# Performance work log

Hardware: AMD Instinct MI355X
Metric: run time of the kernel (lower is better)

Reference implementation:

```python
import jax, jax.numpy as jnp
import numpy as np
import math

N_LABELS = 63          # hard-coded in the original module (view(-1,63), range(63))
IN_DIMS = 8192
OUT_DIMS = 8192


def setup_inputs() -> dict:
    key = jax.random.key(0)
    k1, k2, k3 = jax.random.split(key, 3)
    Label = jax.random.normal(k1, (N_LABELS, IN_DIMS), dtype=jnp.float32)
    S = jax.random.uniform(k2, (N_LABELS, N_LABELS), dtype=jnp.float32)
    stdv = 1.0 / math.sqrt(IN_DIMS)
    # matches torch init: weight ~ U(-stdv, stdv), bias = 0
    W = jax.random.uniform(k3, (OUT_DIMS, IN_DIMS), dtype=jnp.float32,
                           minval=-stdv, maxval=stdv)
    b = jnp.zeros((OUT_DIMS,), dtype=jnp.float32)
    return {"Label": Label, "S": S, "W": W, "b": b}


def reference(Label, S, W, b):
    # MLP: Linear + ReLU -> (63, out_dims)
    X = jax.nn.relu(Label @ W.T + b)
    # torch .view(-1, 63): row-major reshape to (out_dims, 63) (NOT a transpose)
    ML = X.reshape(OUT_DIMS, N_LABELS)
    # loop i: new_Label[i, k] = sum_j S[i, j] * ML[k, j]  ==  S @ ML.T
    return jnp.einsum('ij,kj->ik', S, ML)  # (63, out_dims)
```

## Files before the change

kernel.cpp:

```cpp
#include <hip/hip_runtime.h>
#include <hip/hip_bf16.h>

#define IN_DIMS  8192
#define OUT_DIMS 8192
#define NLAB     63
#define KS       8
#define KCH      (IN_DIMS / KS)
#define BK       64
#define NT       (KCH / BK)
#define BN       64

#define BUFB     24576
#define AOFF     16384

typedef short  s16x8 __attribute__((ext_vector_type(8)));
typedef float  f32x4 __attribute__((ext_vector_type(4)));
typedef unsigned int u32;

__device__ __forceinline__ void gload16(const void* g, void* l) {
    __builtin_amdgcn_global_load_lds(
        (const __attribute__((address_space(1))) u32*)g,
        (__attribute__((address_space(3))) u32*)l, 16, 0, 0);
}

__device__ __forceinline__ unsigned int rne2(float a, float b) {
    unsigned int ua = __float_as_uint(a), ub = __float_as_uint(b);
    ua += 0x7FFFu + ((ua >> 16) & 1u);
    ub += 0x7FFFu + ((ub >> 16) & 1u);
    return (ua >> 16) | (ub & 0xFFFF0000u);
}

__device__ __forceinline__ s16x8 cvt8(float4 a, float4 b) {
    union { __hip_bfloat162 h[4]; s16x8 v; } u;
    u.h[0] = __float22bfloat162_rn(make_float2(a.x, a.y));
    u.h[1] = __float22bfloat162_rn(make_float2(a.z, a.w));
    u.h[2] = __float22bfloat162_rn(make_float2(b.x, b.y));
    u.h[3] = __float22bfloat162_rn(make_float2(b.z, b.w));
    return u.v;
}

__global__ __launch_bounds__(256) void k_prep(const float* __restrict__ L,
                                              unsigned short* __restrict__ A) {
    int e0 = (blockIdx.x * 256 + threadIdx.x) * 4;
    if (e0 >= 64 * IN_DIMS) return;
    float4 v = make_float4(0.f, 0.f, 0.f, 0.f);
    if (e0 < NLAB * IN_DIMS) v = *(const float4*)(L + e0);
    uint2 o;
    o.x = rne2(v.x, v.y);
    o.y = rne2(v.z, v.w);
    *(uint2*)(A + e0) = o;
}

__global__ __launch_bounds__(256, 3) void k_gemm(const float* __restrict__ W,
                                                 const unsigned short* __restrict__ A,
                                                 float* __restrict__ Xp) {
    extern __shared__ char lds[];
    const int nblk = blockIdx.x & 127;
    const int kspl = blockIdx.x >> 7;
    const int w    = threadIdx.x >> 6;
    const int l    = threadIdx.x & 63;
    const int r    = l & 15;
    const int g    = l >> 4;

    const int n0 = nblk * BN;

    f32x4 acc0 = {0,0,0,0}, acc1 = {0,0,0,0}, acc2 = {0,0,0,0}, acc3 = {0,0,0,0};

    auto stage = [&](int tt, int b) {
        const int k0 = kspl * KCH + tt * BK;
        char* base = lds + b * BUFB;
        #pragma unroll
        for (int i = 0; i < 4; ++i) {
            int j    = w * 4 + i;
            int row  = j * 4 + (l >> 4);
            int slot = (l & 15) ^ (row & 7);
            gload16(W + (long)(n0 + row) * IN_DIMS + k0 + slot * 4,
                    base + j * 1024 + l * 16);
        }
        #pragma unroll
        for (int i = 0; i < 2; ++i) {
            int j2   = w * 2 + i;
            int row  = j2 * 8 + (l >> 3);
            int slot = (l & 7) ^ (l >> 3);
            gload16(A + (long)row * IN_DIMS + k0 + slot * 8,
                    base + AOFF + j2 * 1024 + l * 16);
        }
    };

    stage(0, 0);

    for (int t = 0; t < NT; ++t) {
        if (t + 1 < NT) {
            stage(t + 1, (t + 1) & 1);
            asm volatile("s_waitcnt vmcnt(6)" ::: "memory");
        } else {
            asm volatile("s_waitcnt vmcnt(0)" ::: "memory");
        }
        __builtin_amdgcn_s_barrier();
        asm volatile("" ::: "memory");

        const char* base = lds + (t & 1) * BUFB;
        const float* ldsW = (const float*)base;
        const unsigned short* ldsA = (const unsigned short*)(base + AOFF);
        #pragma unroll
        for (int kk = 0; kk < 2; ++kk) {
            int rowb = w * 16 + r;
            int s0 = (kk * 8 + g * 2    ) ^ (r & 7);
            int s1 = (kk * 8 + g * 2 + 1) ^ (r & 7);
            float4 w0 = *(const float4*)(ldsW + rowb * 64 + s0 * 4);
            float4 w1 = *(const float4*)(ldsW + rowb * 64 + s1 * 4);
            s16x8 bw = cvt8(w0, w1);
            int sa = (kk * 4 + g) ^ (r & 7);
            s16x8 a0 = *(const s16x8*)(ldsA + ( 0 + r) * 64 + sa * 8);
            s16x8 a1 = *(const s16x8*)(ldsA + (16 + r) * 64 + sa * 8);
            s16x8 a2 = *(const s16x8*)(ldsA + (32 + r) * 64 + sa * 8);
            s16x8 a3 = *(const s16x8*)(ldsA + (48 + r) * 64 + sa * 8);
            acc0 = __builtin_amdgcn_mfma_f32_16x16x32_bf16(a0, bw, acc0, 0, 0, 0);
            acc1 = __builtin_amdgcn_mfma_f32_16x16x32_bf16(a1, bw, acc1, 0, 0, 0);
            acc2 = __builtin_amdgcn_mfma_f32_16x16x32_bf16(a2, bw, acc2, 0, 0, 0);
            acc3 = __builtin_amdgcn_mfma_f32_16x16x32_bf16(a3, bw, acc3, 0, 0, 0);
        }
        asm volatile("" ::: "memory");
        __builtin_amdgcn_s_barrier();
    }

    float* xo = Xp + (long)kspl * BN * OUT_DIMS + n0 + w * 16 + r;
    #pragma unroll
    for (int q = 0; q < 4; ++q) {
        int m = g * 4 + q;
        xo[(long)(m     ) * OUT_DIMS] = acc0[q];
        xo[(long)(m + 16) * OUT_DIMS] = acc1[q];
        xo[(long)(m + 32) * OUT_DIMS] = acc2[q];
        xo[(long)(m + 48) * OUT_DIMS] = acc3[q];
    }
}

__global__ __launch_bounds__(256) void k_out(const float* __restrict__ Xp,
                                             const float* __restrict__ S,
                                             const float* __restrict__ b,
                                             float* __restrict__ out) {
    __shared__ float sS[NLAB * NLAB];
    __shared__ float sml[64 * NLAB];
    const int k0 = blockIdx.x * 64;

    for (int p = threadIdx.x; p < NLAB * NLAB; p += 256) sS[p] = S[p];
    for (int p = threadIdx.x; p < 64 * NLAB; p += 256) {
        int gi = k0 * NLAB + p;
        float v = 0.f;
        #pragma unroll
        for (int s = 0; s < KS; ++s)
            v += Xp[(long)s * 64 * OUT_DIMS + gi];
        v += b[gi & (OUT_DIMS - 1)];
        sml[p] = v > 0.f ? v : 0.f;
    }
    __syncthreads();

    for (int p = threadIdx.x; p < NLAB * 64; p += 256) {
        int i  = p >> 6;
        int kk = p & 63;
        const float* srow = &sS[i * NLAB];
        const float* mrow = &sml[kk * NLAB];
        float sum = 0.f;
        #pragma unroll
        for (int j = 0; j < NLAB; ++j) sum += srow[j] * mrow[j];
        out[(long)i * OUT_DIMS + k0 + kk] = sum;
    }
}

extern "C" void kernel_launch(void* const* d_in, const int* in_sizes, int n_in,
                              void* d_out, int out_size, void* d_ws, size_t ws_size,
                              hipStream_t stream) {
    const float* Label = (const float*)d_in[0];
    const float* S     = (const float*)d_in[1];
    const float* W     = (const float*)d_in[2];
    const float* b     = (const float*)d_in[3];
    float* out = (float*)d_out;

    unsigned short* A  = (unsigned short*)d_ws;
    float*          Xp = (float*)((char*)d_ws + 64 * IN_DIMS * 2);

    k_prep<<<dim3((64 * IN_DIMS / 4 + 255) / 256), dim3(256), 0, stream>>>(Label, A);
    k_gemm<<<dim3(128 * KS), dim3(256), 2 * BUFB, stream>>>(W, A, Xp);
    k_out <<<dim3(OUT_DIMS / 64), dim3(256), 0, stream>>>(Xp, S, b, out);
}
```

Measured before the change: 92.00 us.

## Make GEMM waves independent: per-wave W staging, direct A loads, no barriers

Each wave now stages only its own 16 W rows into a private LDS region and reads the bf16 Label operand straight from global memory (L2-resident) instead of sharing it through LDS. This removes both block-wide barriers per k-step, shrinks LDS per block, and raises the occupancy hint to 4 blocks. The last iteration issues a dummy reload of tile 0 to keep a uniform vmcnt count. k_out now uses 32-column blocks for more parallelism. The risk is more global/L2 traffic for A, since every wave refetches it, and higher latency on those loads.

```diff
diff --git a/kernel.cpp b/kernel.cpp
--- a/kernel.cpp
+++ b/kernel.cpp
@@ -9,9 +9,8 @@
 #define BK       64
 #define NT       (KCH / BK)
 #define BN       64
-
-#define BUFB     24576
-#define AOFF     16384
+#define WAVETILE 4096
+#define BUFB     (4 * WAVETILE)
 
 typedef short  s16x8 __attribute__((ext_vector_type(8)));
 typedef float  f32x4 __attribute__((ext_vector_type(4)));
@@ -51,10 +50,10 @@
     *(uint2*)(A + e0) = o;
 }
 
-__global__ __launch_bounds__(256, 3) void k_gemm(const float* __restrict__ W,
+__global__ __launch_bounds__(256, 4) void k_gemm(const float* __restrict__ W,
                                                  const unsigned short* __restrict__ A,
                                                  float* __restrict__ Xp) {
-    extern __shared__ char lds[];
+    __shared__ char lds[2 * BUFB];
     const int nblk = blockIdx.x & 127;
     const int kspl = blockIdx.x >> 7;
     const int w    = threadIdx.x >> 6;
@@ -62,69 +61,59 @@
     const int r    = l & 15;
     const int g    = l >> 4;
 
-    const int n0 = nblk * BN;
+    const int  n0    = nblk * BN + w * 16;
+    const long kbase = (long)kspl * KCH;
+
+    char* wbuf0 = lds + w * WAVETILE;
+    char* wbuf1 = lds + BUFB + w * WAVETILE;
+
+    const int srow  = l >> 4;
+    const int sslot = l & 15;
+
+    auto stage = [&](int tt, char* buf) {
+        const long k0 = kbase + (long)tt * BK;
+        #pragma unroll
+        for (int i = 0; i < 4; ++i) {
+            int row  = i * 4 + srow;
+            int slot = sslot ^ (row & 7);
+            gload16(W + (long)(n0 + row) * IN_DIMS + k0 + slot * 4,
+                    buf + i * 1024 + l * 16);
+        }
+    };
+
+    stage(0, wbuf0);
+
+    const unsigned short* ap = A + (long)r * IN_DIMS + kbase + g * 8;
 
     f32x4 acc0 = {0,0,0,0}, acc1 = {0,0,0,0}, acc2 = {0,0,0,0}, acc3 = {0,0,0,0};
 
-    auto stage = [&](int tt, int b) {
-        const int k0 = kspl * KCH + tt * BK;
-        char* base = lds + b * BUFB;
-        #pragma unroll
-        for (int i = 0; i < 4; ++i) {
-            int j    = w * 4 + i;
-            int row  = j * 4 + (l >> 4);
-            int slot = (l & 15) ^ (row & 7);
-            gload16(W + (long)(n0 + row) * IN_DIMS + k0 + slot * 4,
-                    base + j * 1024 + l * 16);
-        }
-        #pragma unroll
-        for (int i = 0; i < 2; ++i) {
-            int j2   = w * 2 + i;
-            int row  = j2 * 8 + (l >> 3);
-            int slot = (l & 7) ^ (l >> 3);
-            gload16(A + (long)row * IN_DIMS + k0 + slot * 8,
-                    base + AOFF + j2 * 1024 + l * 16);
-        }
-    };
+    #pragma unroll 1
+    for (int t = 0; t < NT; ++t) {
+        int tn = (t + 1 < NT) ? (t + 1) : 0;
+        stage(tn, ((t + 1) & 1) ? wbuf1 : wbuf0);
+        asm volatile("s_waitcnt vmcnt(4)" ::: "memory");
+        __builtin_amdgcn_sched_barrier(0);
 
-    stage(0, 0);
-
-    for (int t = 0; t < NT; ++t) {
-        if (t + 1 < NT) {
-            stage(t + 1, (t + 1) & 1);
-            asm volatile("s_waitcnt vmcnt(6)" ::: "memory");
-        } else {
-            asm volatile("s_waitcnt vmcnt(0)" ::: "memory");
-        }
-        __builtin_amdgcn_s_barrier();
-        asm volatile("" ::: "memory");
-
-        const char* base = lds + (t & 1) * BUFB;
-        const float* ldsW = (const float*)base;
-        const unsigned short* ldsA = (const unsigned short*)(base + AOFF);
+        const float* ldsW = (const float*)((t & 1) ? wbuf1 : wbuf0);
+        const long ka = (long)t * BK;
         #pragma unroll
         for (int kk = 0; kk < 2; ++kk) {
-            int rowb = w * 16 + r;
-            int s0 = (kk * 8 + g * 2    ) ^ (r & 7);
-            int s1 = (kk * 8 + g * 2 + 1) ^ (r & 7);
-            float4 w0 = *(const float4*)(ldsW + rowb * 64 + s0 * 4);
-            float4 w1 = *(const float4*)(ldsW + rowb * 64 + s1 * 4);
+            int s0 = ((kk * 8) + g * 2) ^ (r & 7);
+            float4 w0 = *(const float4*)(ldsW + r * 64 + s0 * 4);
+            float4 w1 = *(const float4*)(ldsW + r * 64 + (s0 ^ 1) * 4);
             s16x8 bw = cvt8(w0, w1);
-            int sa = (kk * 4 + g) ^ (r & 7);
-            s16x8 a0 = *(const s16x8*)(ldsA + ( 0 + r) * 64 + sa * 8);
-            s16x8 a1 = *(const s16x8*)(ldsA + (16 + r) * 64 + sa * 8);
-            s16x8 a2 = *(const s16x8*)(ldsA + (32 + r) * 64 + sa * 8);
-            s16x8 a3 = *(const s16x8*)(ldsA + (48 + r) * 64 + sa * 8);
+            s16x8 a0 = *(const s16x8*)(ap + ka + kk * 32);
+            s16x8 a1 = *(const s16x8*)(ap + ka + kk * 32 + 16L * IN_DIMS);
+            s16x8 a2 = *(const s16x8*)(ap + ka + kk * 32 + 32L * IN_DIMS);
+            s16x8 a3 = *(const s16x8*)(ap + ka + kk * 32 + 48L * IN_DIMS);
             acc0 = __builtin_amdgcn_mfma_f32_16x16x32_bf16(a0, bw, acc0, 0, 0, 0);
             acc1 = __builtin_amdgcn_mfma_f32_16x16x32_bf16(a1, bw, acc1, 0, 0, 0);
             acc2 = __builtin_amdgcn_mfma_f32_16x16x32_bf16(a2, bw, acc2, 0, 0, 0);
             acc3 = __builtin_amdgcn_mfma_f32_16x16x32_bf16(a3, bw, acc3, 0, 0, 0);
         }
-        asm volatile("" ::: "memory");
-        __builtin_amdgcn_s_barrier();
     }
 
-    float* xo = Xp + (long)kspl * BN * OUT_DIMS + n0 + w * 16 + r;
+    float* xo = Xp + (long)kspl * BN * OUT_DIMS + n0 + r;
     #pragma unroll
     for (int q = 0; q < 4; ++q) {
         int m = g * 4 + q;
@@ -140,11 +129,11 @@
                                              const float* __restrict__ b,
                                              float* __restrict__ out) {
     __shared__ float sS[NLAB * NLAB];
-    __shared__ float sml[64 * NLAB];
-    const int k0 = blockIdx.x * 64;
+    __shared__ float sml[32 * NLAB];
+    const int k0 = blockIdx.x * 32;
 
     for (int p = threadIdx.x; p < NLAB * NLAB; p += 256) sS[p] = S[p];
-    for (int p = threadIdx.x; p < 64 * NLAB; p += 256) {
+    for (int p = threadIdx.x; p < 32 * NLAB; p += 256) {
         int gi = k0 * NLAB + p;
         float v = 0.f;
         #pragma unroll
@@ -155,9 +144,9 @@
     }
     __syncthreads();
 
-    for (int p = threadIdx.x; p < NLAB * 64; p += 256) {
-        int i  = p >> 6;
-        int kk = p & 63;
+    for (int p = threadIdx.x; p < NLAB * 32; p += 256) {
+        int i  = p >> 5;
+        int kk = p & 31;
         const float* srow = &sS[i * NLAB];
         const float* mrow = &sml[kk * NLAB];
         float sum = 0.f;
@@ -180,6 +169,6 @@
     float*          Xp = (float*)((char*)d_ws + 64 * IN_DIMS * 2);
 
     k_prep<<<dim3((64 * IN_DIMS / 4 + 255) / 256), dim3(256), 0, stream>>>(Label, A);
-    k_gemm<<<dim3(128 * KS), dim3(256), 2 * BUFB, stream>>>(W, A, Xp);
-    k_out <<<dim3(OUT_DIMS / 64), dim3(256), 0, stream>>>(Xp, S, b, out);
+    k_gemm<<<dim3(128 * KS), dim3(256), 0, stream>>>(W, A, Xp);
+    k_out <<<dim3(OUT_DIMS / 32), dim3(256), 0, stream>>>(Xp, S, b, out);
 }
```

Measured after the change: 104.7 us. 13.8% more time.
